# Performance work log

Hardware: AMD Instinct MI355X
Metric: run time of the kernel (lower is better)

## Reference

```python
import jax, jax.numpy as jnp
import numpy as np

H = 512       # hidden size
NL = 2        # GRU layers
LAM = 0.01
F = 81919     # freq_size
C = 16384     # c_size (number of frequency groups)
G = 5         # group_size
NIN = 5       # x + 4 extra inputs (the reshape hardcodes 5)
FP = C * G    # padded freq size = 81920
RP, LP = 0, 1 # pad split so FP - F = 1


def cplx(a):
    return jax.lax.complex(a[..., 0], a[..., 1])


def csig(z):
    # split-activation complex sigmoid (MetaAF complex_utils)
    return jax.lax.complex(jax.nn.sigmoid(z.real), jax.nn.sigmoid(z.imag))


def ctanh(z):
    return jax.lax.complex(jnp.tanh(z.real), jnp.tanh(z.imag))


def cgru_cell(x, state, w_i, w_h, b):
    # Complex GRU cell; same wiring as hk.GRU but with complex weights
    # and split real/imag sigmoid/tanh gates.
    h = state.shape[-1]
    gates_x = x @ w_i                                   # (C, 3H)
    zr_x, a_x = gates_x[:, :2 * h], gates_x[:, 2 * h:]
    zr = csig(zr_x + state @ w_h[:, :2 * h] + b[:2 * h])
    z, r = zr[:, :h], zr[:, h:]
    a = ctanh(a_x + (r * state) @ w_h[:, 2 * h:] + b[2 * h:])
    return (1 - z) * state + z * a


def _forward(x, extras, h, w_in, b_in, w_i, w_h, b_rnn, w_out, b_out):
    # x: (1,F,1) complex; extras: (4,1,F,1) complex; h: (NL,C,H) complex
    stack = jnp.concatenate([x[..., None], jnp.moveaxis(extras, 0, -1)], axis=-1)  # (1,F,1,5)
    # log1p magnitude compression, phase preserved
    stack = jnp.log1p(jnp.abs(stack)) * jnp.exp(1j * jnp.angle(stack))
    # pad freq dim to FP (rp left, lp right) -- matches the pad+slice trick
    stack = jnp.pad(stack, ((0, 0), (RP, LP), (0, 0), (0, 0)))                     # (1,FP,1,5)
    rnn_in = stack.reshape(C, NIN * G) @ w_in + b_in                               # (C,H) in_lin
    cur = rnn_in
    new_h = []
    for l in range(NL):
        cur = cgru_cell(cur, h[l], w_i[l], w_h[l], b_rnn[l])
        new_h.append(cur)
    y = cur @ w_out + b_out                                                        # (C,G) out_lin
    y = y.reshape(1, FP, 1, 1)[:, :F]                                              # drop pad
    out = -LAM * y[..., 0]                                                         # (1,F,1)
    return out, jnp.stack(new_h)


def setup_inputs():
    key = jax.random.key(0)
    ks = jax.random.split(key, 8)
    rn = lambda k, s, sc=1.0: jax.random.normal(k, s, dtype=jnp.float32) * sc
    return {
        "x_ri": rn(ks[0], (1, F, 1, 2)),
        "extras_ri": rn(ks[1], (4, 1, F, 1, 2)),
        "h_ri": rn(ks[2], (NL, C, H, 2), 0.1),
        "w_in_ri": rn(ks[3], (NIN * G, H, 2), (2.0 * NIN * G) ** -0.5),
        "b_in_ri": jnp.zeros((H, 2), jnp.float32),
        "w_i_ri": rn(ks[4], (NL, H, 3 * H, 2), (2.0 * H) ** -0.5),
        "w_h_ri": rn(ks[5], (NL, H, 3 * H, 2), (2.0 * H) ** -0.5),
        "b_rnn_ri": jnp.zeros((NL, 3 * H, 2), jnp.float32),
        "w_out_ri": rn(ks[6], (H, G, 2), (2.0 * H) ** -0.5),
        "b_out_ri": jnp.zeros((G, 2), jnp.float32),
    }


def reference(x_ri, extras_ri, h_ri, w_in_ri, b_in_ri, w_i_ri, w_h_ri, b_rnn_ri, w_out_ri, b_out_ri):
    args = [cplx(a) for a in (x_ri, extras_ri, h_ri, w_in_ri, b_in_ri,
                              w_i_ri, w_h_ri, b_rnn_ri, w_out_ri, b_out_ri)]
    return _forward(*args)
```

## Files before the change

kernel.cpp:

```cpp
#include <hip/hip_runtime.h>
#include <math.h>

#define FF   81919
#define CC   16384
#define HH   512
#define NLL  2
#define GG   5
#define LAMF 0.01f

#define CH   (CC * HH)

typedef short short8 __attribute__((ext_vector_type(8)));
typedef float f32x4  __attribute__((ext_vector_type(4)));

#define W_IN_E_SZ  (1024 * 64)
#define W_ZR_SZ    (2048 * 2048)
#define W_A_SZ     (1024 * 2048)
#define W_TOTAL_SH (W_IN_E_SZ + 2 * W_ZR_SZ + 2 * W_A_SZ)

__device__ __forceinline__ float sigmoidf_(float x) { return 1.0f / (1.0f + expf(-x)); }
__device__ __forceinline__ unsigned short f2bf(float f) {
    unsigned u = __float_as_uint(f);
    u = (u + 0x7FFF + ((u >> 16) & 1)) >> 16;
    return (unsigned short)u;
}
__device__ __forceinline__ float bf2f(unsigned short u) {
    return __uint_as_float(((unsigned)u) << 16);
}
__device__ __forceinline__ void gld_lds16(const unsigned short* g, unsigned short* l) {
    __builtin_amdgcn_global_load_lds(
        (const __attribute__((address_space(1))) void*)g,
        (__attribute__((address_space(3))) void*)l, 16, 0, 0);
}

__global__ __launch_bounds__(256) void expand_in(const float2* __restrict__ w,
                                                 unsigned short* __restrict__ Bt) {
    int i = blockIdx.x * 256 + threadIdx.x;
    if (i >= 512 * 4) return;
    int n = i & 511, kg = i >> 9;
    unsigned short r0[16], r1[16];
#pragma unroll
    for (int j = 0; j < 8; j++) {
        int kc = kg * 8 + j;
        float re = 0.f, im = 0.f;
        if (kc < 25) { float2 v = w[(size_t)kc * 512 + n]; re = v.x; im = v.y; }
        r0[2 * j] = f2bf(re);  r0[2 * j + 1] = f2bf(-im);
        r1[2 * j] = f2bf(im);  r1[2 * j + 1] = f2bf(re);
    }
    unsigned short* p0 = Bt + (size_t)(2 * n) * 64 + kg * 16;
    unsigned short* p1 = Bt + (size_t)(2 * n + 1) * 64 + kg * 16;
#pragma unroll
    for (int q = 0; q < 2; q++) {
        ((uint4*)p0)[q] = ((uint4*)r0)[q];
        ((uint4*)p1)[q] = ((uint4*)r1)[q];
    }
}

__global__ __launch_bounds__(256) void expand2(const float2* __restrict__ src0,
                                               const float2* __restrict__ src1,
                                               int Nc,
                                               unsigned short* __restrict__ Bt) {
    int total = Nc * 2 * 64;
    int i = blockIdx.x * 256 + threadIdx.x;
    if (i >= total) return;
    int kg = i / (2 * Nc);
    int rem = i - kg * 2 * Nc;
    int part = rem / Nc, n = rem - part * Nc;
    const float2* src = part ? src1 : src0;
    unsigned short r0[16], r1[16];
#pragma unroll
    for (int j = 0; j < 8; j++) {
        int kc = kg * 8 + j;
        float2 v = src[(size_t)kc * 1536 + n];
        r0[2 * j] = f2bf(v.x);  r0[2 * j + 1] = f2bf(-v.y);
        r1[2 * j] = f2bf(v.y);  r1[2 * j + 1] = f2bf(v.x);
    }
    size_t ko = (size_t)part * 1024 + kg * 16;
    unsigned short* p0 = Bt + (size_t)(2 * n) * 2048 + ko;
    unsigned short* p1 = Bt + (size_t)(2 * n + 1) * 2048 + ko;
#pragma unroll
    for (int q = 0; q < 2; q++) {
        ((uint4*)p0)[q] = ((uint4*)r0)[q];
        ((uint4*)p1)[q] = ((uint4*)r1)[q];
    }
}

__global__ __launch_bounds__(256) void prep_kernel(const float2* __restrict__ x,
                                                   const float2* __restrict__ extras,
                                                   unsigned short* __restrict__ stk,
                                                   int r0, int m) {
    int i = blockIdx.x * 256 + threadIdx.x;
    if (i >= m * 32) return;
    int c = i >> 5, j = i & 31;
    float2 o = make_float2(0.f, 0.f);
    if (j < 25) {
        int g = j / 5, n = j - g * 5;
        int pos = (r0 + c) * 5 + g;
        float2 v = make_float2(0.f, 0.f);
        if (pos < FF) v = (n == 0) ? x[pos] : extras[(size_t)(n - 1) * FF + pos];
        float r = sqrtf(v.x * v.x + v.y * v.y);
        float sc = (r > 0.f) ? (log1pf(r) / r) : 0.f;
        o = make_float2(v.x * sc, v.y * sc);
    }
    stk[(size_t)c * 64 + 2 * j]     = f2bf(o.x);
    stk[(size_t)c * 64 + 2 * j + 1] = f2bf(o.y);
}

__global__ __launch_bounds__(256) void cvt_state(const float* __restrict__ hf,
                                                 unsigned short* __restrict__ XS,
                                                 int r0, int m) {
    int i = blockIdx.x * 256 + threadIdx.x;
    if (i >= m * 128) return;
    int c = i >> 7, q = i & 127;
    const float4* s = (const float4*)(hf + (size_t)(r0 + c) * 1024 + q * 8);
    float4 a = s[0], b = s[1];
    short8 o;
    o[0] = f2bf(a.x); o[1] = f2bf(a.y); o[2] = f2bf(a.z); o[3] = f2bf(a.w);
    o[4] = f2bf(b.x); o[5] = f2bf(b.y); o[6] = f2bf(b.z); o[7] = f2bf(b.w);
    *(short8*)(XS + (size_t)c * 3072 + q * 8) = o;
}

#define EPI_BF16 0
#define EPI_ZR   2
#define EPI_A    3

template <int EPI>
__global__ __launch_bounds__(512, 2) void gemm256(const unsigned short* __restrict__ A, int lda,
                                                  const unsigned short* __restrict__ Bt, int ldb,
                                                  const float* __restrict__ bias,
                                                  unsigned short* __restrict__ Cb, int ldc,
                                                  float* __restrict__ Zbuf,
                                                  const float* __restrict__ hf,
                                                  unsigned short* __restrict__ XS,
                                                  float* __restrict__ hr,
                                                  int rowoff, int nk) {
    __shared__ __align__(16) unsigned short LA[4][8192];
    __shared__ __align__(16) unsigned short LB[4][8192];

    int t = threadIdx.x, lane = t & 63, w = t >> 6;

    int nbx = gridDim.x;
    int nwg = nbx * gridDim.y;
    int id = blockIdx.y * nbx + blockIdx.x;
    int cpx = nwg >> 3;
    id = (id & 7) * cpx + (id >> 3);
    int m0 = (id / nbx) * 256, n0 = (id % nbx) * 256;

    int wr = w >> 2, wc = w & 3;
    int cl = lane & 15, rg = lane >> 4;

    int lrow = lane >> 2;
    int lcol = ((lane & 3) ^ ((lane >> 3) & 3)) * 8;
    const unsigned short* AgS0 = A  + (size_t)(m0 + w * 32 + lrow) * lda + lcol;
    const unsigned short* AgS1 = A  + (size_t)(m0 + w * 32 + 16 + lrow) * lda + lcol;
    const unsigned short* BgS0 = Bt + (size_t)(n0 + w * 32 + lrow) * ldb + lcol;
    const unsigned short* BgS1 = Bt + (size_t)(n0 + w * 32 + 16 + lrow) * ldb + lcol;

#define STAGE_A(b, j) do { int _o = (j) * 32;                         \
        gld_lds16(AgS0 + _o, &LA[b][w * 1024]);                        \
        gld_lds16(AgS1 + _o, &LA[b][w * 1024 + 512]); } while (0)
#define STAGE_B(b, j) do { int _o = (j) * 32;                         \
        gld_lds16(BgS0 + _o, &LB[b][w * 1024]);                        \
        gld_lds16(BgS1 + _o, &LB[b][w * 1024 + 512]); } while (0)

    if (nk > 0) { STAGE_A(0, 0); STAGE_B(0, 0); }
    if (nk > 1) { STAGE_A(1, 1); STAGE_B(1, 1); }
    if (nk > 2) { STAGE_A(2, 2); STAGE_B(2, 2); }

    int sA = (rg ^ ((cl >> 1) & 3)) * 8;

    f32x4 acc[8][4] = {};

    for (int kt = 0; kt < nk; kt++) {
        if (kt < nk - 2)       asm volatile("s_waitcnt vmcnt(8)" ::: "memory");
        else if (kt == nk - 2) asm volatile("s_waitcnt vmcnt(4)" ::: "memory");
        else                   asm volatile("s_waitcnt vmcnt(0)" ::: "memory");
        __builtin_amdgcn_s_barrier();

        int b = kt & 3;
        const unsigned short* Ab = LA[b];
        const unsigned short* Bb = LB[b];

        short8 bf[4], af[4];
#pragma unroll
        for (int ni = 0; ni < 4; ni++)
            bf[ni] = *(const short8*)&Bb[(wc * 64 + ni * 16 + cl) * 32 + sA];
#pragma unroll
        for (int mi = 0; mi < 4; mi++)
            af[mi] = *(const short8*)&Ab[(wr * 128 + mi * 16 + cl) * 32 + sA];
        if (kt + 3 < nk) STAGE_A((kt + 3) & 3, kt + 3);
        __builtin_amdgcn_s_barrier();
        __builtin_amdgcn_s_setprio(1);
#pragma unroll
        for (int mi = 0; mi < 4; mi++)
#pragma unroll
            for (int ni = 0; ni < 4; ni++)
                acc[mi][ni] = __builtin_amdgcn_mfma_f32_16x16x32_bf16(
                    af[mi], bf[ni], acc[mi][ni], 0, 0, 0);
        __builtin_amdgcn_s_setprio(0);
        __builtin_amdgcn_s_barrier();

#pragma unroll
        for (int mi = 0; mi < 4; mi++)
            af[mi] = *(const short8*)&Ab[(wr * 128 + (mi + 4) * 16 + cl) * 32 + sA];
        if (kt + 3 < nk) STAGE_B((kt + 3) & 3, kt + 3);
        __builtin_amdgcn_s_barrier();
        __builtin_amdgcn_s_setprio(1);
#pragma unroll
        for (int mi = 0; mi < 4; mi++)
#pragma unroll
            for (int ni = 0; ni < 4; ni++)
                acc[mi + 4][ni] = __builtin_amdgcn_mfma_f32_16x16x32_bf16(
                    af[mi], bf[ni], acc[mi + 4][ni], 0, 0, 0);
        __builtin_amdgcn_s_setprio(0);
    }
#undef STAGE_A
#undef STAGE_B

    int odd = lane & 1;
#pragma unroll
    for (int ni = 0; ni < 4; ni++) {
        int col = n0 + wc * 64 + ni * 16 + cl;
        float bv = bias[col];
#pragma unroll
        for (int mi = 0; mi < 8; mi++) {
#pragma unroll
            for (int r = 0; r < 4; r++) {
                int row = m0 + wr * 128 + mi * 16 + rg * 4 + r;
                float v = acc[mi][ni][r] + bv;
                if (EPI == EPI_BF16) {
                    Cb[(size_t)row * ldc + col] = f2bf(v);
                } else if (EPI == EPI_ZR) {
                    float sv = sigmoidf_(v);
                    if (col < 1024) {
                        Zbuf[(size_t)row * 1024 + col] = sv;
                    } else {
                        float pv = __shfl_xor(sv, 1);
                        int k = (col >> 1) - 512;
                        float2 s = *(const float2*)&hf[(size_t)(rowoff + row) * 1024 + 2 * k];
                        float o = odd ? (pv * s.y + sv * s.x)
                                      : (sv * s.x - pv * s.y);
                        XS[(size_t)row * 3072 + 1024 + col] = f2bf(o);
                    }
                } else {
                    float tv = tanhf(v);
                    float pt = __shfl_xor(tv, 1);
                    int k = col >> 1;
                    float2 z = *(const float2*)&Zbuf[(size_t)row * 1024 + 2 * k];
                    float2 s = *(const float2*)&hf[(size_t)(rowoff + row) * 1024 + 2 * k];
                    float o;
                    if (odd) o = (1.f - z.x) * s.y - z.y * s.x + z.x * tv + z.y * pt;
                    else     o = (1.f - z.x) * s.x + z.y * s.y + z.x * tv - z.y * pt;
                    XS[(size_t)row * 3072 + 1024 + col] = f2bf(o);
                    if (!odd) hr[(size_t)(rowoff + row) * 512 + k] = o;
                }
            }
        }
    }
}

__global__ __launch_bounds__(256) void outmm_kernel(const unsigned short* __restrict__ XS,
                                                    const float2* __restrict__ w_out,
                                                    const float2* __restrict__ b_out,
                                                    float* __restrict__ out,
                                                    int r0, int m) {
    int wid = (blockIdx.x * 256 + threadIdx.x) >> 6;
    int lane = threadIdx.x & 63;
    if (wid >= m * GG) return;
    int c = wid / GG, g = wid - c * GG;
    const unsigned short* arow = XS + (size_t)c * 3072 + 1024;
    float ax = 0.f;
    for (int k = lane; k < HH; k += 64) {
        unsigned u = *(const unsigned*)(arow + 2 * k);
        float vx = bf2f((unsigned short)(u & 0xffff));
        float vy = bf2f((unsigned short)(u >> 16));
        float2 wv = w_out[k * GG + g];
        ax += vx * wv.x - vy * wv.y;
    }
#pragma unroll
    for (int off = 32; off > 0; off >>= 1) ax += __shfl_down(ax, off);
    if (lane == 0) {
        int p = (r0 + c) * GG + g;
        if (p < FF) out[p] = -LAMF * (ax + b_out[g].x);
    }
}

extern "C" void kernel_launch(void* const* d_in, const int* in_sizes, int n_in,
                              void* d_out, int out_size, void* d_ws, size_t ws_size,
                              hipStream_t stream) {
    const float2* x      = (const float2*)d_in[0];
    const float2* extras = (const float2*)d_in[1];
    const float2* h      = (const float2*)d_in[2];
    const float2* w_in   = (const float2*)d_in[3];
    const float2* b_in   = (const float2*)d_in[4];
    const float2* w_i    = (const float2*)d_in[5];
    const float2* w_h    = (const float2*)d_in[6];
    const float2* b_rnn  = (const float2*)d_in[7];
    const float2* w_out  = (const float2*)d_in[8];
    const float2* b_out  = (const float2*)d_in[9];

    float* outf   = (float*)d_out;
    float* houtr0 = outf + FF;
    float* houtr1 = houtr0 + (size_t)CH;

    unsigned short* wsh    = (unsigned short*)d_ws;
    unsigned short* w_in_e = wsh;
    unsigned short* bzr0   = w_in_e + W_IN_E_SZ;
    unsigned short* bzr1   = bzr0 + W_ZR_SZ;
    unsigned short* ba0    = bzr1 + W_ZR_SZ;
    unsigned short* ba1    = ba0 + W_A_SZ;

    size_t wbytes = (size_t)W_TOTAL_SH * 2;
    int chunk = CC;
    while (chunk > 1024 && wbytes + (size_t)chunk * 10368 > ws_size) chunk >>= 1;
    int nch = CC / chunk;

    unsigned short* XS  = ba1 + W_A_SZ;
    unsigned short* stk = XS + (size_t)chunk * 3072;
    float*          Zb  = (float*)(stk + (size_t)chunk * 64);

    expand_in<<<(512 * 4 + 255) / 256, 256, 0, stream>>>(w_in, w_in_e);
    for (int l = 0; l < NLL; l++) {
        const float2* wil = w_i + (size_t)l * HH * 1536;
        const float2* whl = w_h + (size_t)l * HH * 1536;
        expand2<<<(1024 * 2 * 64 + 255) / 256, 256, 0, stream>>>(whl, wil, 1024, l ? bzr1 : bzr0);
        expand2<<<(512 * 2 * 64 + 255) / 256, 256, 0, stream>>>(wil + 1024, whl + 1024, 512, l ? ba1 : ba0);
    }

    for (int cb = 0; cb < nch; cb++) {
        int r0 = cb * chunk;
        int gy = chunk / 256;

        prep_kernel<<<(chunk * 32 + 255) / 256, 256, 0, stream>>>(x, extras, stk, r0, chunk);
        gemm256<EPI_BF16><<<dim3(4, gy), 512, 0, stream>>>(
            stk, 64, w_in_e, 64, (const float*)b_in,
            XS + 1024, 3072, nullptr, nullptr, nullptr, nullptr, 0, 2);

        for (int l = 0; l < NLL; l++) {
            const float* hf = (const float*)(h + (size_t)l * CH);
            const float* bl = (const float*)(b_rnn + (size_t)l * 1536);
            float* hr = (l == 0) ? houtr0 : houtr1;
            const unsigned short* bzr = l ? bzr1 : bzr0;
            const unsigned short* ba  = l ? ba1 : ba0;

            cvt_state<<<chunk * 128 / 256, 256, 0, stream>>>(hf, XS, r0, chunk);
            gemm256<EPI_ZR><<<dim3(8, gy), 512, 0, stream>>>(
                XS, 3072, bzr, 2048, bl,
                nullptr, 0, Zb, hf, XS, nullptr, r0, 64);
            gemm256<EPI_A><<<dim3(4, gy), 512, 0, stream>>>(
                XS + 1024, 3072, ba, 2048, bl + 2048,
                nullptr, 0, Zb, hf, XS, hr, r0, 64);
        }

        outmm_kernel<<<(chunk * GG * 64 + 255) / 256, 256, 0, stream>>>(
            XS, w_out, b_out, outf, r0, chunk);
    }
}
```

Baseline: 1.095 ms.

## Switch GEMM mainloop to double-buffered K=64 tiles with one barrier per step

Replaces the 4-stage, K=32-per-step LDS pipeline with a 2-buffer scheme where each iteration stages a K=64 tile (two K=32 subtiles) and waits with vmcnt(0) at a single barrier. This cuts the number of barriers and loop iterations per K and loads all 8 A fragments at once. In exchange, prefetch depth drops from three tiles ahead to one, so global-load latency is less hidden. More A fragments live in registers at once, which may raise register pressure under the 2-block occupancy bound.

```diff
diff --git a/kernel.cpp b/kernel.cpp
--- a/kernel.cpp
+++ b/kernel.cpp
@@ -133,9 +133,9 @@
                                                   const float* __restrict__ hf,
                                                   unsigned short* __restrict__ XS,
                                                   float* __restrict__ hr,
-                                                  int rowoff, int nk) {
-    __shared__ __align__(16) unsigned short LA[4][8192];
-    __shared__ __align__(16) unsigned short LB[4][8192];
+                                                  int rowoff, int nt) {
+    __shared__ __align__(16) unsigned short LA[2][2][8192];
+    __shared__ __align__(16) unsigned short LB[2][2][8192];
 
     int t = threadIdx.x, lane = t & 63, w = t >> 6;
 
@@ -156,66 +156,53 @@
     const unsigned short* BgS0 = Bt + (size_t)(n0 + w * 32 + lrow) * ldb + lcol;
     const unsigned short* BgS1 = Bt + (size_t)(n0 + w * 32 + 16 + lrow) * ldb + lcol;
 
-#define STAGE_A(b, j) do { int _o = (j) * 32;                         \
-        gld_lds16(AgS0 + _o, &LA[b][w * 1024]);                        \
-        gld_lds16(AgS1 + _o, &LA[b][w * 1024 + 512]); } while (0)
-#define STAGE_B(b, j) do { int _o = (j) * 32;                         \
-        gld_lds16(BgS0 + _o, &LB[b][w * 1024]);                        \
-        gld_lds16(BgS1 + _o, &LB[b][w * 1024 + 512]); } while (0)
-
-    if (nk > 0) { STAGE_A(0, 0); STAGE_B(0, 0); }
-    if (nk > 1) { STAGE_A(1, 1); STAGE_B(1, 1); }
-    if (nk > 2) { STAGE_A(2, 2); STAGE_B(2, 2); }
+#define STAGE(b, tt)                                                   \
+    do {                                                               \
+        _Pragma("unroll")                                              \
+        for (int _kk = 0; _kk < 2; _kk++) {                            \
+            int _o = (tt) * 64 + _kk * 32;                             \
+            gld_lds16(AgS0 + _o, &LA[b][_kk][w * 1024]);               \
+            gld_lds16(AgS1 + _o, &LA[b][_kk][w * 1024 + 512]);         \
+            gld_lds16(BgS0 + _o, &LB[b][_kk][w * 1024]);               \
+            gld_lds16(BgS1 + _o, &LB[b][_kk][w * 1024 + 512]);         \
+        }                                                              \
+    } while (0)
 
     int sA = (rg ^ ((cl >> 1) & 3)) * 8;
 
     f32x4 acc[8][4] = {};
 
-    for (int kt = 0; kt < nk; kt++) {
-        if (kt < nk - 2)       asm volatile("s_waitcnt vmcnt(8)" ::: "memory");
-        else if (kt == nk - 2) asm volatile("s_waitcnt vmcnt(4)" ::: "memory");
-        else                   asm volatile("s_waitcnt vmcnt(0)" ::: "memory");
+    STAGE(0, 0);
+
+    int buf = 0;
+    for (int kt = 0; kt < nt; kt++) {
+        asm volatile("s_waitcnt vmcnt(0)" ::: "memory");
         __builtin_amdgcn_s_barrier();
-
-        int b = kt & 3;
-        const unsigned short* Ab = LA[b];
-        const unsigned short* Bb = LB[b];
-
-        short8 bf[4], af[4];
-#pragma unroll
-        for (int ni = 0; ni < 4; ni++)
-            bf[ni] = *(const short8*)&Bb[(wc * 64 + ni * 16 + cl) * 32 + sA];
-#pragma unroll
-        for (int mi = 0; mi < 4; mi++)
-            af[mi] = *(const short8*)&Ab[(wr * 128 + mi * 16 + cl) * 32 + sA];
-        if (kt + 3 < nk) STAGE_A((kt + 3) & 3, kt + 3);
-        __builtin_amdgcn_s_barrier();
-        __builtin_amdgcn_s_setprio(1);
-#pragma unroll
-        for (int mi = 0; mi < 4; mi++)
+        if (kt + 1 < nt) STAGE(buf ^ 1, kt + 1);
+
+#pragma unroll
+        for (int kk = 0; kk < 2; kk++) {
+            const unsigned short* Ab = &LA[buf][kk][0];
+            const unsigned short* Bb = &LB[buf][kk][0];
+            short8 af[8], bf[4];
 #pragma unroll
             for (int ni = 0; ni < 4; ni++)
-                acc[mi][ni] = __builtin_amdgcn_mfma_f32_16x16x32_bf16(
-                    af[mi], bf[ni], acc[mi][ni], 0, 0, 0);
-        __builtin_amdgcn_s_setprio(0);
-        __builtin_amdgcn_s_barrier();
-
-#pragma unroll
-        for (int mi = 0; mi < 4; mi++)
-            af[mi] = *(const short8*)&Ab[(wr * 128 + (mi + 4) * 16 + cl) * 32 + sA];
-        if (kt + 3 < nk) STAGE_B((kt + 3) & 3, kt + 3);
-        __builtin_amdgcn_s_barrier();
-        __builtin_amdgcn_s_setprio(1);
-#pragma unroll
-        for (int mi = 0; mi < 4; mi++)
-#pragma unroll
-            for (int ni = 0; ni < 4; ni++)
-                acc[mi + 4][ni] = __builtin_amdgcn_mfma_f32_16x16x32_bf16(
-                    af[mi], bf[ni], acc[mi + 4][ni], 0, 0, 0);
-        __builtin_amdgcn_s_setprio(0);
-    }
-#undef STAGE_A
-#undef STAGE_B
+                bf[ni] = *(const short8*)&Bb[(wc * 64 + ni * 16 + cl) * 32 + sA];
+#pragma unroll
+            for (int mi = 0; mi < 8; mi++)
+                af[mi] = *(const short8*)&Ab[(wr * 128 + mi * 16 + cl) * 32 + sA];
+            __builtin_amdgcn_s_setprio(1);
+#pragma unroll
+            for (int mi = 0; mi < 8; mi++)
+#pragma unroll
+                for (int ni = 0; ni < 4; ni++)
+                    acc[mi][ni] = __builtin_amdgcn_mfma_f32_16x16x32_bf16(
+                        af[mi], bf[ni], acc[mi][ni], 0, 0, 0);
+            __builtin_amdgcn_s_setprio(0);
+        }
+        buf ^= 1;
+    }
+#undef STAGE
 
     int odd = lane & 1;
 #pragma unroll
@@ -334,7 +321,7 @@
         prep_kernel<<<(chunk * 32 + 255) / 256, 256, 0, stream>>>(x, extras, stk, r0, chunk);
         gemm256<EPI_BF16><<<dim3(4, gy), 512, 0, stream>>>(
             stk, 64, w_in_e, 64, (const float*)b_in,
-            XS + 1024, 3072, nullptr, nullptr, nullptr, nullptr, 0, 2);
+            XS + 1024, 3072, nullptr, nullptr, nullptr, nullptr, 0, 1);
 
         for (int l = 0; l < NLL; l++) {
             const float* hf = (const float*)(h + (size_t)l * CH);
@@ -346,10 +333,10 @@
             cvt_state<<<chunk * 128 / 256, 256, 0, stream>>>(hf, XS, r0, chunk);
             gemm256<EPI_ZR><<<dim3(8, gy), 512, 0, stream>>>(
                 XS, 3072, bzr, 2048, bl,
-                nullptr, 0, Zb, hf, XS, nullptr, r0, 64);
+                nullptr, 0, Zb, hf, XS, nullptr, r0, 32);
             gemm256<EPI_A><<<dim3(4, gy), 512, 0, stream>>>(
                 XS + 1024, 3072, ba, 2048, bl + 2048,
-                nullptr, 0, Zb, hf, XS, hr, r0, 64);
+                nullptr, 0, Zb, hf, XS, hr, r0, 32);
         }
 
         outmm_kernel<<<(chunk * GG * 64 + 255) / 256, 256, 0, stream>>>(
```

After: 1.136 ms. +3.7%, slower.
